# Kernel optimization log

Measured on AMD Instinct MI355X. Metric: run time of the kernel, lower is better.

Reference implementation:

```python
import jax, jax.numpy as jnp
import numpy as np

NUM_REF = 20
LINE_SCORE_THRESH = 0.6
MIN_PLANE_AREA = 100
H, W, N_LINES = 480, 640, 100


def _sobel(x):
    # x: [B,1,H,W] -> [B,2,H,W]; standard Sobel edge conv (kx, ky), padding=1
    kx = jnp.array([[1., 0., -1.], [2., 0., -2.], [1., 0., -1.]], x.dtype)
    ky = jnp.array([[1., 2., 1.], [0., 0., 0.], [-1., -2., -1.]], x.dtype)
    k = jnp.stack([kx, ky])[:, None]  # [2,1,3,3]
    return jax.lax.conv_general_dilated(x, k, (1, 1), [(1, 1), (1, 1)],
                                         dimension_numbers=('NCHW', 'OIHW', 'NCHW'))


def setup_inputs() -> dict:
    key = jax.random.key(0)
    k1, k2, k3, k4, k5 = jax.random.split(key, 5)
    depth_pred = jax.random.normal(k1, (1, 1, H, W), jnp.float32)
    depth_gt = jax.random.uniform(k2, (1, 1, H, W), jnp.float32)
    line_pred = jax.random.uniform(k3, (1, N_LINES, 6), jnp.float32)
    line_score = jax.random.normal(k4, (1, N_LINES, 2), jnp.float32)
    valid_mask = jax.random.randint(k5, (1, 1, H, W), 0, 2) > 0
    return {"depth_pred": depth_pred, "depth_gt": depth_gt,
            "line_pred": line_pred, "line_score": line_score,
            "valid_mask": valid_mask}


def reference(depth_pred, depth_gt, line_pred, line_score, valid_mask):
    h, w = depth_pred.shape[-2:]
    # how many lines pass the softmax threshold -> number of planes actually used
    probs = jax.nn.softmax(line_score, axis=-1)
    num_kept = jnp.sum(probs[0, :, 0] > LINE_SCORE_THRESH)
    top_num = jnp.minimum(num_kept, NUM_REF)
    # top-k by raw class-0 logit (torch.topk is sorted, so top `top_num` = prefix)
    _, t_ids = jax.lax.top_k(line_score[0, :, 0], NUM_REF)
    chosen = line_pred[0][t_ids]  # [P,6]
    scale = jnp.array([w, h, w, h, w, h], jnp.float32)
    xy = jnp.round(chosen * scale).reshape(NUM_REF, 3, 2)  # [P,3,(x,y)]
    xy = jnp.stack([jnp.clip(xy[..., 0], 0, w - 1),
                    jnp.clip(xy[..., 1], 0, h - 1)], axis=-1)
    # Sobel normal map
    g = _sobel(depth_pred)              # [1,2,H,W]
    nx, ny = -g[0, 0], -g[0, 1]          # [H,W]
    valid = valid_mask[0, 0]             # [H,W] bool
    # vectorized point-in-triangle: cross-product sign test for all P planes
    px = jnp.arange(w, dtype=jnp.float32).reshape(1, 1, 1, w)
    py = jnp.arange(h, dtype=jnp.float32).reshape(1, 1, h, 1)
    nxt = xy[:, jnp.array([1, 2, 0])]
    ex = (nxt[..., 0] - xy[..., 0])[..., None, None]  # [P,3,1,1]
    ey = (nxt[..., 1] - xy[..., 1])[..., None, None]
    vx = xy[..., 0][..., None, None]
    vy = xy[..., 1][..., None, None]
    d = ex * (py - vy) - ey * (px - vx)               # [P,3,H,W]
    inside = jnp.all(d >= 0, axis=1) | jnp.all(d <= 0, axis=1)  # [P,H,W]
    m = inside & valid
    cnt = jnp.sum(m, axis=(1, 2)).astype(jnp.float32)  # [P]
    safe = jnp.maximum(cnt, 1.0)
    mf = m.astype(nx.dtype)
    mean_x = jnp.sum(mf * nx, axis=(1, 2)) / safe
    mean_y = jnp.sum(mf * ny, axis=(1, 2)) / safe
    var_x = jnp.sum(mf * (nx - mean_x[:, None, None]) ** 2, axis=(1, 2)) / safe
    var_y = jnp.sum(mf * (ny - mean_y[:, None, None]) ** 2, axis=(1, 2)) / safe
    include = (cnt >= MIN_PLANE_AREA) & (jnp.arange(NUM_REF) < top_num)
    total = jnp.maximum(jnp.sum(include), 1).astype(jnp.float32)
    loss_var = jnp.sum(jnp.where(include, var_x + var_y, 0.0)) / total
    return loss_var
```

## Files before the change

### kernel.cpp

```cpp
#include <hip/hip_runtime.h>
#include <math.h>

#define HH 480
#define WW 640
#define NL 100
#define NREF 20

#define FLAGS_OFF 240
#define PART_OFF 512

__global__ void plane_setup_kernel(const float* __restrict__ line_pred,
                                   const float* __restrict__ line_score,
                                   float* __restrict__ w) {
    __shared__ float s_sc[NL];
    __shared__ int s_flags[NL];
    __shared__ int s_topnum;
    int i = threadIdx.x;

    float s0 = 0.0f;
    if (i < NL) {
        s0 = line_score[2 * i];
        float s1 = line_score[2 * i + 1];
        s_sc[i] = s0;
        float p0 = 1.0f / (1.0f + expf(s1 - s0));
        s_flags[i] = (p0 > 0.6f) ? 1 : 0;
    }
    __syncthreads();
    if (i == 0) {
        int nk = 0;
        for (int j = 0; j < NL; j++) nk += s_flags[j];
        s_topnum = (nk < NREF) ? nk : NREF;
    }
    __syncthreads();

    if (i < NL) {
        int rank = 0;
        for (int j = 0; j < NL; j++) {
            float sj = s_sc[j];
            rank += ((sj > s0) || (sj == s0 && j < i)) ? 1 : 0;
        }
        if (rank < NREF) {
            float c[6];
            #pragma unroll
            for (int q = 0; q < 6; q++) c[q] = line_pred[6 * i + q];
            float vx[3], vy[3];
            #pragma unroll
            for (int v = 0; v < 3; v++) {
                float x = rintf(c[2 * v] * (float)WW);
                float y = rintf(c[2 * v + 1] * (float)HH);
                vx[v] = fminf(fmaxf(x, 0.0f), (float)(WW - 1));
                vy[v] = fminf(fmaxf(y, 0.0f), (float)(HH - 1));
            }
            float* td = w + rank * 12;
            #pragma unroll
            for (int e = 0; e < 3; e++) {
                int n = (e + 1) % 3;
                td[e * 4 + 0] = vx[n] - vx[e];
                td[e * 4 + 1] = vy[n] - vy[e];
                td[e * 4 + 2] = vx[e];
                td[e * 4 + 3] = vy[e];
            }
            w[FLAGS_OFF + rank] = (rank < s_topnum) ? 1.0f : 0.0f;
        }
    }
}

__global__ __launch_bounds__(256) void plane_main_kernel(
    const float* __restrict__ depth, const int* __restrict__ valid,
    float* __restrict__ w) {
    __shared__ float ds[3 * WW];
    __shared__ int vsh[WW];
    __shared__ float tri8[NREF * 8];

    const int r = blockIdx.x;
    const int tid = threadIdx.x;
    const float py = (float)r;

    for (int idx = tid; idx < 3 * (WW / 4); idx += 256) {
        const int lr = idx / (WW / 4);
        const int c4 = idx - lr * (WW / 4);
        const int g = r - 1 + lr;
        float4 v = make_float4(0.f, 0.f, 0.f, 0.f);
        if ((unsigned)g < (unsigned)HH) v = ((const float4*)depth)[g * (WW / 4) + c4];
        ((float4*)ds)[idx] = v;
    }
    for (int idx = tid; idx < WW / 4; idx += 256)
        ((int4*)vsh)[idx] = ((const int4*)valid)[r * (WW / 4) + idx];
    if (tid < NREF * 3) {
        const int t = tid / 3, e = tid - 3 * t;
        const float* td = w + t * 12 + e * 4;
        const float ex = td[0], eyv = td[1], vx = td[2], vy = td[3];
        tri8[t * 8 + e * 2]     = fmaf(ex, py - vy, eyv * vx);
        tri8[t * 8 + e * 2 + 1] = eyv;
    }
    __syncthreads();

    const int wid = tid >> 6, lane = tid & 63;
    float ae[5][3], ey[5][3];
    #pragma unroll
    for (int i = 0; i < 5; i++)
        #pragma unroll
        for (int e = 0; e < 3; e++) {
            ae[i][e] = tri8[(wid * 5 + i) * 8 + e * 2];
            ey[i][e] = tri8[(wid * 5 + i) * 8 + e * 2 + 1];
        }

    float acc[5][4];
    #pragma unroll
    for (int i = 0; i < 5; i++)
        #pragma unroll
        for (int q = 0; q < 4; q++) acc[i][q] = 0.f;

    #pragma unroll
    for (int j = 0; j < 10; j++) {
        const int x = j * 64 + lane;
        const float px = (float)x;
        const float fl = (x > 0) ? 1.f : 0.f;
        const float fr = (x < WW - 1) ? 1.f : 0.f;
        const int xm = x - (x > 0), xp = x + (x < WW - 1);
        const float a00 = ds[xm] * fl,          a01 = ds[x],          a02 = ds[xp] * fr;
        const float a10 = ds[WW + xm] * fl,                           a12 = ds[WW + xp] * fr;
        const float a20 = ds[2 * WW + xm] * fl, a21 = ds[2 * WW + x], a22 = ds[2 * WW + xp] * fr;
        const float gx = (a00 - a02) + 2.f * (a10 - a12) + (a20 - a22);
        const float gy = (a00 + 2.f * a01 + a02) - (a20 + 2.f * a21 + a22);
        const float nx = -gx, ny = -gy;
        const float s2 = nx * nx + ny * ny;
        const bool vm = (vsh[x] != 0);
        #pragma unroll
        for (int i = 0; i < 5; i++) {
            const float d0 = fmaf(-ey[i][0], px, ae[i][0]);
            const float d1 = fmaf(-ey[i][1], px, ae[i][1]);
            const float d2 = fmaf(-ey[i][2], px, ae[i][2]);
            const float dmin = fminf(fminf(d0, d1), d2);
            const float dmax = fmaxf(fmaxf(d0, d1), d2);
            const bool m = ((dmin >= 0.f) | (dmax <= 0.f)) & vm;
            const float mf = m ? 1.f : 0.f;
            acc[i][0] += mf;
            acc[i][1] = fmaf(mf, nx, acc[i][1]);
            acc[i][2] = fmaf(mf, ny, acc[i][2]);
            acc[i][3] = fmaf(mf, s2, acc[i][3]);
        }
    }

    #pragma unroll
    for (int off = 32; off > 0; off >>= 1)
        #pragma unroll
        for (int i = 0; i < 5; i++)
            #pragma unroll
            for (int q = 0; q < 4; q++)
                acc[i][q] += __shfl_down(acc[i][q], off);
    if (lane == 0) {
        #pragma unroll
        for (int i = 0; i < 5; i++)
            #pragma unroll
            for (int q = 0; q < 4; q++)
                w[PART_OFF + ((wid * 5 + i) * 4 + q) * HH + r] = acc[i][q];
    }
}

__global__ __launch_bounds__(128) void plane_finalize_kernel(
    const float* __restrict__ w, float* __restrict__ out) {
    __shared__ float s_col[NREF * 4];
    const int tid = threadIdx.x;
    if (tid < NREF * 4) {
        const float4* col = (const float4*)(w + PART_OFF + tid * HH);
        float4 s4 = make_float4(0.f, 0.f, 0.f, 0.f);
        #pragma unroll 8
        for (int p = 0; p < HH / 4; p++) {
            float4 v = col[p];
            s4.x += v.x; s4.y += v.y; s4.z += v.z; s4.w += v.w;
        }
        s_col[tid] = (s4.x + s4.y) + (s4.z + s4.w);
    }
    __syncthreads();
    float val = 0.f, inc = 0.f;
    if (tid < NREF) {
        const float c  = s_col[tid * 4 + 0];
        const float sx = s_col[tid * 4 + 1];
        const float sy = s_col[tid * 4 + 2];
        const float sq = s_col[tid * 4 + 3];
        const float safe = fmaxf(c, 1.f);
        const float mx = sx / safe, my = sy / safe;
        const float var = (sq - 2.f * mx * sx - 2.f * my * sy
                           + c * (mx * mx + my * my)) / safe;
        inc = (c >= 100.f) ? w[FLAGS_OFF + tid] : 0.f;
        val = inc * var;
    }
    if (tid < 64) {
        #pragma unroll
        for (int off = 32; off > 0; off >>= 1) {
            val += __shfl_down(val, off);
            inc += __shfl_down(inc, off);
        }
        if (tid == 0) out[0] = val / fmaxf(inc, 1.f);
    }
}

extern "C" void kernel_launch(void* const* d_in, const int* in_sizes, int n_in,
                              void* d_out, int out_size, void* d_ws, size_t ws_size,
                              hipStream_t stream) {
    const float* depth_pred = (const float*)d_in[0];
    const float* line_pred  = (const float*)d_in[2];
    const float* line_score = (const float*)d_in[3];
    const int*   valid_mask = (const int*)d_in[4];
    float* out = (float*)d_out;
    float* w = (float*)d_ws;

    plane_setup_kernel<<<1, 128, 0, stream>>>(line_pred, line_score, w);
    plane_main_kernel<<<HH, 256, 0, stream>>>(depth_pred, valid_mask, w);
    plane_finalize_kernel<<<1, 128, 0, stream>>>(w, out);
}
```

Baseline: 83.57 us.

## Fuse plane setup into main kernel and process two rows per block

```diff
diff --git a/kernel.cpp b/kernel.cpp
--- a/kernel.cpp
+++ b/kernel.cpp
@@ -5,105 +5,77 @@
 #define WW 640
 #define NL 100
 #define NREF 20
-
-#define FLAGS_OFF 240
-#define PART_OFF 512
-
-__global__ void plane_setup_kernel(const float* __restrict__ line_pred,
-                                   const float* __restrict__ line_score,
-                                   float* __restrict__ w) {
-    __shared__ float s_sc[NL];
-    __shared__ int s_flags[NL];
-    __shared__ int s_topnum;
-    int i = threadIdx.x;
-
-    float s0 = 0.0f;
-    if (i < NL) {
-        s0 = line_score[2 * i];
-        float s1 = line_score[2 * i + 1];
-        s_sc[i] = s0;
-        float p0 = 1.0f / (1.0f + expf(s1 - s0));
-        s_flags[i] = (p0 > 0.6f) ? 1 : 0;
-    }
-    __syncthreads();
-    if (i == 0) {
-        int nk = 0;
-        for (int j = 0; j < NL; j++) nk += s_flags[j];
-        s_topnum = (nk < NREF) ? nk : NREF;
-    }
-    __syncthreads();
-
-    if (i < NL) {
-        int rank = 0;
-        for (int j = 0; j < NL; j++) {
-            float sj = s_sc[j];
-            rank += ((sj > s0) || (sj == s0 && j < i)) ? 1 : 0;
-        }
-        if (rank < NREF) {
-            float c[6];
-            #pragma unroll
-            for (int q = 0; q < 6; q++) c[q] = line_pred[6 * i + q];
-            float vx[3], vy[3];
-            #pragma unroll
-            for (int v = 0; v < 3; v++) {
-                float x = rintf(c[2 * v] * (float)WW);
-                float y = rintf(c[2 * v + 1] * (float)HH);
-                vx[v] = fminf(fmaxf(x, 0.0f), (float)(WW - 1));
-                vy[v] = fminf(fmaxf(y, 0.0f), (float)(HH - 1));
-            }
-            float* td = w + rank * 12;
-            #pragma unroll
-            for (int e = 0; e < 3; e++) {
-                int n = (e + 1) % 3;
-                td[e * 4 + 0] = vx[n] - vx[e];
-                td[e * 4 + 1] = vy[n] - vy[e];
-                td[e * 4 + 2] = vx[e];
-                td[e * 4 + 3] = vy[e];
-            }
-            w[FLAGS_OFF + rank] = (rank < s_topnum) ? 1.0f : 0.0f;
-        }
-    }
-}
+#define RPB 2
+#define NB (HH / RPB)
+
 
 __global__ __launch_bounds__(256) void plane_main_kernel(
     const float* __restrict__ depth, const int* __restrict__ valid,
+    const float* __restrict__ line_pred, const float* __restrict__ line_score,
     float* __restrict__ w) {
-    __shared__ float ds[3 * WW];
-    __shared__ int vsh[WW];
-    __shared__ float tri8[NREF * 8];
-
-    const int r = blockIdx.x;
+    __shared__ float ds[(RPB + 2) * WW];
+    __shared__ int vsh[RPB * WW];
+    __shared__ float s_sc[NL];
+    __shared__ float s_vert[NREF][6];
+    __shared__ float s_ae[RPB][NREF * 3];
+    __shared__ float s_ey[NREF * 3];
+
     const int tid = threadIdx.x;
-    const float py = (float)r;
-
-    for (int idx = tid; idx < 3 * (WW / 4); idx += 256) {
+    const int base = blockIdx.x * RPB;
+
+    if (tid < NL) s_sc[tid] = ((const float2*)line_score)[tid].x;
+
+    for (int idx = tid; idx < (RPB + 2) * (WW / 4); idx += 256) {
         const int lr = idx / (WW / 4);
         const int c4 = idx - lr * (WW / 4);
-        const int g = r - 1 + lr;
+        const int g = base - 1 + lr;
         float4 v = make_float4(0.f, 0.f, 0.f, 0.f);
         if ((unsigned)g < (unsigned)HH) v = ((const float4*)depth)[g * (WW / 4) + c4];
         ((float4*)ds)[idx] = v;
     }
-    for (int idx = tid; idx < WW / 4; idx += 256)
-        ((int4*)vsh)[idx] = ((const int4*)valid)[r * (WW / 4) + idx];
+    for (int idx = tid; idx < RPB * (WW / 4); idx += 256)
+        ((int4*)vsh)[idx] = ((const int4*)valid)[base * (WW / 4) + idx];
+    __syncthreads();
+
+    if (tid < NL) {
+        const float s0 = s_sc[tid];
+        int rank = 0;
+        for (int j = 0; j < NL; j++) {
+            const float sj = s_sc[j];
+            rank += ((sj > s0) || (sj == s0 && j < tid)) ? 1 : 0;
+        }
+        if (rank < NREF) {
+            const float2 c01 = ((const float2*)line_pred)[3 * tid];
+            const float2 c23 = ((const float2*)line_pred)[3 * tid + 1];
+            const float2 c45 = ((const float2*)line_pred)[3 * tid + 2];
+            s_vert[rank][0] = fminf(fmaxf(rintf(c01.x * (float)WW), 0.f), (float)(WW - 1));
+            s_vert[rank][1] = fminf(fmaxf(rintf(c01.y * (float)HH), 0.f), (float)(HH - 1));
+            s_vert[rank][2] = fminf(fmaxf(rintf(c23.x * (float)WW), 0.f), (float)(WW - 1));
+            s_vert[rank][3] = fminf(fmaxf(rintf(c23.y * (float)HH), 0.f), (float)(HH - 1));
+            s_vert[rank][4] = fminf(fmaxf(rintf(c45.x * (float)WW), 0.f), (float)(WW - 1));
+            s_vert[rank][5] = fminf(fmaxf(rintf(c45.y * (float)HH), 0.f), (float)(HH - 1));
+        }
+    }
+    __syncthreads();
+
     if (tid < NREF * 3) {
-        const int t = tid / 3, e = tid - 3 * t;
-        const float* td = w + t * 12 + e * 4;
-        const float ex = td[0], eyv = td[1], vx = td[2], vy = td[3];
-        tri8[t * 8 + e * 2]     = fmaf(ex, py - vy, eyv * vx);
-        tri8[t * 8 + e * 2 + 1] = eyv;
+        const int t = tid / 3, e = tid - 3 * t, n = (e + 1) % 3;
+        const float vx = s_vert[t][2 * e], vy = s_vert[t][2 * e + 1];
+        const float ex = s_vert[t][2 * n] - vx, eyv = s_vert[t][2 * n + 1] - vy;
+        s_ey[tid] = eyv;
+        #pragma unroll
+        for (int rr = 0; rr < RPB; rr++)
+            s_ae[rr][tid] = fmaf(ex, (float)(base + rr) - vy, eyv * vx);
     }
     __syncthreads();
 
     const int wid = tid >> 6, lane = tid & 63;
-    float ae[5][3], ey[5][3];
+    float eyr[5][3];
     #pragma unroll
     for (int i = 0; i < 5; i++)
         #pragma unroll
-        for (int e = 0; e < 3; e++) {
-            ae[i][e] = tri8[(wid * 5 + i) * 8 + e * 2];
-            ey[i][e] = tri8[(wid * 5 + i) * 8 + e * 2 + 1];
-        }
+        for (int e = 0; e < 3; e++)
+            eyr[i][e] = s_ey[(wid * 5 + i) * 3 + e];
 
     float acc[5][4];
     #pragma unroll
@@ -112,33 +84,46 @@
         for (int q = 0; q < 4; q++) acc[i][q] = 0.f;
 
     #pragma unroll
-    for (int j = 0; j < 10; j++) {
-        const int x = j * 64 + lane;
-        const float px = (float)x;
-        const float fl = (x > 0) ? 1.f : 0.f;
-        const float fr = (x < WW - 1) ? 1.f : 0.f;
-        const int xm = x - (x > 0), xp = x + (x < WW - 1);
-        const float a00 = ds[xm] * fl,          a01 = ds[x],          a02 = ds[xp] * fr;
-        const float a10 = ds[WW + xm] * fl,                           a12 = ds[WW + xp] * fr;
-        const float a20 = ds[2 * WW + xm] * fl, a21 = ds[2 * WW + x], a22 = ds[2 * WW + xp] * fr;
-        const float gx = (a00 - a02) + 2.f * (a10 - a12) + (a20 - a22);
-        const float gy = (a00 + 2.f * a01 + a02) - (a20 + 2.f * a21 + a22);
-        const float nx = -gx, ny = -gy;
-        const float s2 = nx * nx + ny * ny;
-        const bool vm = (vsh[x] != 0);
-        #pragma unroll
-        for (int i = 0; i < 5; i++) {
-            const float d0 = fmaf(-ey[i][0], px, ae[i][0]);
-            const float d1 = fmaf(-ey[i][1], px, ae[i][1]);
-            const float d2 = fmaf(-ey[i][2], px, ae[i][2]);
-            const float dmin = fminf(fminf(d0, d1), d2);
-            const float dmax = fmaxf(fmaxf(d0, d1), d2);
-            const bool m = ((dmin >= 0.f) | (dmax <= 0.f)) & vm;
-            const float mf = m ? 1.f : 0.f;
-            acc[i][0] += mf;
-            acc[i][1] = fmaf(mf, nx, acc[i][1]);
-            acc[i][2] = fmaf(mf, ny, acc[i][2]);
-            acc[i][3] = fmaf(mf, s2, acc[i][3]);
+    for (int rr = 0; rr < RPB; rr++) {
+        float ae[5][3];
+        #pragma unroll
+        for (int i = 0; i < 5; i++)
+            #pragma unroll
+            for (int e = 0; e < 3; e++)
+                ae[i][e] = s_ae[rr][(wid * 5 + i) * 3 + e];
+        const float* rm = ds + rr * WW;
+        const float* rc = ds + (rr + 1) * WW;
+        const float* rp = ds + (rr + 2) * WW;
+        const int* vrow = vsh + rr * WW;
+        #pragma unroll
+        for (int j = 0; j < 10; j++) {
+            const int x = j * 64 + lane;
+            const float px = (float)x;
+            const float fl = (x > 0) ? 1.f : 0.f;
+            const float fr = (x < WW - 1) ? 1.f : 0.f;
+            const int xm = x - (x > 0), xp = x + (x < WW - 1);
+            const float a00 = rm[xm] * fl, a01 = rm[x], a02 = rm[xp] * fr;
+            const float a10 = rc[xm] * fl,               a12 = rc[xp] * fr;
+            const float a20 = rp[xm] * fl, a21 = rp[x], a22 = rp[xp] * fr;
+            const float gx = (a00 - a02) + 2.f * (a10 - a12) + (a20 - a22);
+            const float gy = (a00 + 2.f * a01 + a02) - (a20 + 2.f * a21 + a22);
+            const float nx = -gx, ny = -gy;
+            const float s2 = nx * nx + ny * ny;
+            const bool vm = (vrow[x] != 0);
+            #pragma unroll
+            for (int i = 0; i < 5; i++) {
+                const float d0 = fmaf(-eyr[i][0], px, ae[i][0]);
+                const float d1 = fmaf(-eyr[i][1], px, ae[i][1]);
+                const float d2 = fmaf(-eyr[i][2], px, ae[i][2]);
+                const float dmin = fminf(fminf(d0, d1), d2);
+                const float dmax = fmaxf(fmaxf(d0, d1), d2);
+                const bool m = ((dmin >= 0.f) | (dmax <= 0.f)) & vm;
+                const float mf = m ? 1.f : 0.f;
+                acc[i][0] += mf;
+                acc[i][1] = fmaf(mf, nx, acc[i][1]);
+                acc[i][2] = fmaf(mf, ny, acc[i][2]);
+                acc[i][3] = fmaf(mf, s2, acc[i][3]);
+            }
         }
     }
 
@@ -154,25 +139,40 @@
         for (int i = 0; i < 5; i++)
             #pragma unroll
             for (int q = 0; q < 4; q++)
-                w[PART_OFF + ((wid * 5 + i) * 4 + q) * HH + r] = acc[i][q];
+                w[((wid * 5 + i) * 4 + q) * NB + blockIdx.x] = acc[i][q];
     }
 }
 
 __global__ __launch_bounds__(128) void plane_finalize_kernel(
-    const float* __restrict__ w, float* __restrict__ out) {
+    const float* __restrict__ line_score, const float* __restrict__ w,
+    float* __restrict__ out) {
     __shared__ float s_col[NREF * 4];
+    __shared__ int s_cnt[2];
     const int tid = threadIdx.x;
+    const int lane = tid & 63, wid = tid >> 6;
+
+    int flag = 0;
+    if (tid < NL) {
+        const float2 sc = ((const float2*)line_score)[tid];
+        const float p0 = 1.0f / (1.0f + expf(sc.y - sc.x));
+        flag = (p0 > 0.6f) ? 1 : 0;
+    }
+    const unsigned long long b = __ballot(flag);
+    if (lane == 0) s_cnt[wid] = __popcll(b);
+
     if (tid < NREF * 4) {
-        const float4* col = (const float4*)(w + PART_OFF + tid * HH);
+        const float4* col = (const float4*)(w + tid * NB);
         float4 s4 = make_float4(0.f, 0.f, 0.f, 0.f);
-        #pragma unroll 8
-        for (int p = 0; p < HH / 4; p++) {
-            float4 v = col[p];
+        #pragma unroll 4
+        for (int p = 0; p < NB / 4; p++) {
+            const float4 v = col[p];
             s4.x += v.x; s4.y += v.y; s4.z += v.z; s4.w += v.w;
         }
         s_col[tid] = (s4.x + s4.y) + (s4.z + s4.w);
     }
     __syncthreads();
+
+    const int topnum = min(s_cnt[0] + s_cnt[1], NREF);
     float val = 0.f, inc = 0.f;
     if (tid < NREF) {
         const float c  = s_col[tid * 4 + 0];
@@ -183,7 +183,7 @@
         const float mx = sx / safe, my = sy / safe;
         const float var = (sq - 2.f * mx * sx - 2.f * my * sy
                            + c * (mx * mx + my * my)) / safe;
-        inc = (c >= 100.f) ? w[FLAGS_OFF + tid] : 0.f;
+        inc = ((c >= 100.f) && (tid < topnum)) ? 1.f : 0.f;
         val = inc * var;
     }
     if (tid < 64) {
@@ -206,7 +206,7 @@
     float* out = (float*)d_out;
     float* w = (float*)d_ws;
 
-    plane_setup_kernel<<<1, 128, 0, stream>>>(line_pred, line_score, w);
-    plane_main_kernel<<<HH, 256, 0, stream>>>(depth_pred, valid_mask, w);
-    plane_finalize_kernel<<<1, 128, 0, stream>>>(w, out);
+    plane_main_kernel<<<NB, 256, 0, stream>>>(depth_pred, valid_mask,
+                                              line_pred, line_score, w);
+    plane_finalize_kernel<<<1, 128, 0, stream>>>(line_score, w, out);
 }
```

Measured after the change: 78.79 us (median of 2 runs). 5.7% less time.
